# Kernel optimization log

Hardware: AMD Instinct MI355X
Metric: run time of the kernel (lower is better)

Reference implementation:

```python
import jax, jax.numpy as jnp
import numpy as np

# QConv2D (AngleMap feature map, entanglement-free PQC model):
# each 3x3 patch value x_q is angle-encoded as RY(w_q * x_q) on qubit q,
# then n_layers of trainable RZ(a)/RY(b) rotations are applied; the layer
# outputs the Bloch vector (<X>,<Y>,<Z>) of every qubit -> 3*n_qubits values
# per patch. Channel outputs are summed (Add), filters concatenated, relu.

KERNEL = (3, 3)
STRIDE = (1, 1)


def _extract_patches(x, k, s):
    # x: (B,H,W,C) -> (B,i0,i1,C,K) with K = k0*k1
    B, H, W, C = x.shape
    i0 = (H - k[0]) // s[0] + 1
    i1 = (W - k[1]) // s[1] + 1
    ri = jnp.arange(i0)[:, None] * s[0] + jnp.arange(k[0])[None, :]  # (i0,k0)
    rj = jnp.arange(i1)[:, None] * s[1] + jnp.arange(k[1])[None, :]  # (i1,k1)
    p = x[:, ri]            # (B,i0,k0,W,C)
    p = p[:, :, :, rj]      # (B,i0,k0,i1,k1,C)
    p = jnp.transpose(p, (0, 1, 3, 5, 2, 4))  # (B,i0,i1,C,k0,k1)
    return p.reshape(B, i0, i1, C, k[0] * k[1])


def setup_inputs() -> dict:
    key = jax.random.key(0)
    k_x, k_w, k_a, k_b = jax.random.split(key, 4)
    B, H, W, C = 32, 128, 128, 3
    F, Q, L = 2, KERNEL[0] * KERNEL[1], 2  # filters, n_qubits, n_layers
    input_tensor = jax.random.uniform(k_x, (B, H, W, C), dtype=jnp.float32)
    w_enc = jax.random.normal(k_w, (F, C, Q), dtype=jnp.float32)
    a_rz = jax.random.normal(k_a, (F, C, L, Q), dtype=jnp.float32)
    b_ry = jax.random.normal(k_b, (F, C, L, Q), dtype=jnp.float32)
    return {"input_tensor": input_tensor, "w_enc": w_enc, "a_rz": a_rz, "b_ry": b_ry}


def reference(input_tensor, w_enc, a_rz, b_ry):
    B = input_tensor.shape[0]
    F, C, Q = w_enc.shape
    L = a_rz.shape[2]
    patches = _extract_patches(input_tensor, KERNEL, STRIDE)  # (B,i0,i1,C,Q)
    i0, i1 = patches.shape[1], patches.shape[2]
    # angle encoding per (filter, channel, qubit)
    theta = patches[:, :, :, None, :, :] * w_enc[None, None, None]  # (B,i0,i1,F,C,Q)
    vx, vy, vz = jnp.sin(theta), jnp.zeros_like(theta), jnp.cos(theta)
    for l in range(L):  # small fixed layer count
        ca, sa = jnp.cos(a_rz[:, :, l]), jnp.sin(a_rz[:, :, l])  # (F,C,Q)
        cb, sb = jnp.cos(b_ry[:, :, l]), jnp.sin(b_ry[:, :, l])
        # RZ(a): rotate Bloch vector about Z
        vx, vy = vx * ca - vy * sa, vx * sa + vy * ca
        # RY(b): rotate about Y
        vx, vz = vx * cb + vz * sb, -vx * sb + vz * cb
    out = jnp.stack([vx, vy, vz], axis=-1)       # (B,i0,i1,F,C,Q,3)
    out = out.sum(axis=4)                        # Add over channels -> (B,i0,i1,F,Q,3)
    out = out.reshape(B, i0, i1, F * Q * 3)      # Concatenate over filters
    return jax.nn.relu(out)
```

## Files before the change

kernel.cpp:

```cpp
#include <hip/hip_runtime.h>
#include <math.h>

#define NB 32
#define NH 128
#define NW 128
#define NC 3
#define NF 2
#define NQ 9
#define NL 2
#define I0 126
#define I1 126
#define NGJ 14
#define NGROUPS (NB * I0 * NGJ)
#define GTHREADS (NGROUPS * 18)
#define INV2PI 0.15915494309189535f

struct f3 { float x, y, z; };

__global__ __launch_bounds__(256) void qconv_fused(
        const float* __restrict__ x,
        const float* __restrict__ w_enc,
        const float* __restrict__ a_rz,
        const float* __restrict__ b_ry,
        float* __restrict__ out) {
    __shared__ float stab[54 * 8];
    int tid = threadIdx.x;
    if (tid < 54) {
        int t = tid;
        int f = t / 27;
        int c = (t / 9) % 3;
        int q = t % 9;
        float ux = 1.f, uy = 0.f, uz = 0.f;
        float wx = 0.f, wy = 0.f, wz = 1.f;
#pragma unroll
        for (int l = 0; l < NL; ++l) {
            int ia = ((f * NC + c) * NL + l) * NQ + q;
            float sa, ca, sb, cb;
            __sincosf(a_rz[ia], &sa, &ca);
            __sincosf(b_ry[ia], &sb, &cb);
            float nx, ny, nz;
            nx = ux * ca - uy * sa; ny = ux * sa + uy * ca; ux = nx; uy = ny;
            nx = ux * cb + uz * sb; nz = -ux * sb + uz * cb; ux = nx; uz = nz;
            nx = wx * ca - wy * sa; ny = wx * sa + wy * ca; wx = nx; wy = ny;
            nx = wx * cb + wz * sb; nz = -wx * sb + wz * cb; wx = nx; wz = nz;
        }
        float* o = stab + t * 8;
        o[0] = w_enc[t] * INV2PI;
        o[1] = ux; o[2] = uy; o[3] = uz;
        o[4] = wx; o[5] = wy; o[6] = wz;
        o[7] = 0.f;
    }
    __syncthreads();

    int T0 = blockIdx.x * 256 + tid;
    int grp = T0 / 18;
    int q18 = T0 - grp * 18;
    int f = (q18 >= 9) ? 1 : 0;
    int q = q18 - f * 9;
    int di = q / 3, dj = q - di * 3;

    float cw[3], sx[3], sy[3], sz[3], cx[3], cy[3], cz[3];
#pragma unroll
    for (int c = 0; c < 3; ++c) {
        const float* r = stab + (size_t)(f * 27 + c * 9 + q) * 8;
        float4 v0 = *reinterpret_cast<const float4*>(r);
        float4 v1 = *reinterpret_cast<const float4*>(r + 4);
        cw[c] = v0.x; sx[c] = v0.y; sy[c] = v0.z; sz[c] = v0.w;
        cx[c] = v1.x; cy[c] = v1.y; cz[c] = v1.z;
    }

    int b   = grp / (I0 * NGJ);
    int rem = grp - b * (I0 * NGJ);
    int i   = rem / NGJ;
    int j   = (rem - i * NGJ) * 9;

    const float* pin = x + ((size_t)((b * NH + i + di) * NW) + (j + dj)) * NC;
    float* pout = out + (size_t)grp * 486 + q18 * 3;

    float p[27];
#pragma unroll
    for (int t = 0; t < 9; ++t) {
        f3 v = *reinterpret_cast<const f3*>(pin + t * 3);
        p[3 * t + 0] = v.x; p[3 * t + 1] = v.y; p[3 * t + 2] = v.z;
    }

#pragma unroll
    for (int t = 0; t < 9; ++t) {
        float a0 = 0.f, a1 = 0.f, a2 = 0.f;
#pragma unroll
        for (int c = 0; c < 3; ++c) {
            float xr = p[3 * t + c] * cw[c];
            float s  = __builtin_amdgcn_sinf(xr);
            float co = __builtin_amdgcn_cosf(xr);
            a0 = fmaf(sx[c], s, fmaf(cx[c], co, a0));
            a1 = fmaf(sy[c], s, fmaf(cy[c], co, a1));
            a2 = fmaf(sz[c], s, fmaf(cz[c], co, a2));
        }
        f3 r;
        r.x = fmaxf(a0, 0.f);
        r.y = fmaxf(a1, 0.f);
        r.z = fmaxf(a2, 0.f);
        *reinterpret_cast<f3*>(pout + t * 54) = r;
    }
}

extern "C" void kernel_launch(void* const* d_in, const int* in_sizes, int n_in,
                              void* d_out, int out_size, void* d_ws, size_t ws_size,
                              hipStream_t stream) {
    const float* x     = (const float*)d_in[0];
    const float* w_enc = (const float*)d_in[1];
    const float* a_rz  = (const float*)d_in[2];
    const float* b_ry  = (const float*)d_in[3];
    float* out = (float*)d_out;

    int block = 256;
    int grid = GTHREADS / block;
    qconv_fused<<<grid, block, 0, stream>>>(x, w_enc, a_rz, b_ry, out);
}
```

Before: 27.02 us.

## Stage outputs in shared memory and write coalesced nontemporal float4 stores

Reorganizes the thread mapping so each 576-thread block handles 128 output pixels. Each thread owns one (filter,qubit) pair and computes 4 pixels, then writes its results to shared memory. After a barrier, the block writes the contiguous output tile with float4 nontemporal stores. The goal is to replace strided 12-byte scattered writes with fully coalesced wide stores. In exchange, input reads become per-pixel strided loads, and the kernel adds shared-memory traffic and a block barrier.

```diff
diff --git a/kernel.cpp b/kernel.cpp
--- a/kernel.cpp
+++ b/kernel.cpp
@@ -10,20 +10,24 @@
 #define NL 2
 #define I0 126
 #define I1 126
-#define NGJ 14
-#define NGROUPS (NB * I0 * NGJ)
-#define GTHREADS (NGROUPS * 18)
+#define NPIX (NB * I0 * I1)
+#define PPB 128
+#define TPB 576
+#define NBLK (NPIX / PPB)
 #define INV2PI 0.15915494309189535f
 
 struct f3 { float x, y, z; };
+typedef float f4 __attribute__((ext_vector_type(4)));
 
-__global__ __launch_bounds__(256) void qconv_fused(
+__global__ __launch_bounds__(TPB) void qconv_fused(
         const float* __restrict__ x,
         const float* __restrict__ w_enc,
         const float* __restrict__ a_rz,
         const float* __restrict__ b_ry,
         float* __restrict__ out) {
     __shared__ float stab[54 * 8];
+    __shared__ float sout[PPB * 54];
+
     int tid = threadIdx.x;
     if (tid < 54) {
         int t = tid;
@@ -52,9 +56,8 @@
     }
     __syncthreads();
 
-    int T0 = blockIdx.x * 256 + tid;
-    int grp = T0 / 18;
-    int q18 = T0 - grp * 18;
+    int q18 = tid >> 5;
+    int pxl = tid & 31;
     int f = (q18 >= 9) ? 1 : 0;
     int q = q18 - f * 9;
     int di = q / 3, dj = q - di * 3;
@@ -69,38 +72,43 @@
         cx[c] = v1.x; cy[c] = v1.y; cz[c] = v1.z;
     }
 
-    int b   = grp / (I0 * NGJ);
-    int rem = grp - b * (I0 * NGJ);
-    int i   = rem / NGJ;
-    int j   = (rem - i * NGJ) * 9;
-
-    const float* pin = x + ((size_t)((b * NH + i + di) * NW) + (j + dj)) * NC;
-    float* pout = out + (size_t)grp * 486 + q18 * 3;
-
-    float p[27];
-#pragma unroll
-    for (int t = 0; t < 9; ++t) {
-        f3 v = *reinterpret_cast<const f3*>(pin + t * 3);
-        p[3 * t + 0] = v.x; p[3 * t + 1] = v.y; p[3 * t + 2] = v.z;
-    }
+    int pixbase = blockIdx.x * PPB;
 
 #pragma unroll
-    for (int t = 0; t < 9; ++t) {
+    for (int k = 0; k < 4; ++k) {
+        int px  = pixbase + pxl + 32 * k;
+        int b   = px / (I0 * I1);
+        int rem = px - b * (I0 * I1);
+        int i   = rem / I1;
+        int j   = rem - i * I1;
+
+        const float* pp = x + ((size_t)((b * NH + i + di) * NW) + (j + dj)) * NC;
+        f3 P = *reinterpret_cast<const f3*>(pp);
+
         float a0 = 0.f, a1 = 0.f, a2 = 0.f;
 #pragma unroll
         for (int c = 0; c < 3; ++c) {
-            float xr = p[3 * t + c] * cw[c];
+            float pc = (c == 0) ? P.x : (c == 1) ? P.y : P.z;
+            float xr = pc * cw[c];
             float s  = __builtin_amdgcn_sinf(xr);
             float co = __builtin_amdgcn_cosf(xr);
             a0 = fmaf(sx[c], s, fmaf(cx[c], co, a0));
             a1 = fmaf(sy[c], s, fmaf(cy[c], co, a1));
             a2 = fmaf(sz[c], s, fmaf(cz[c], co, a2));
         }
-        f3 r;
-        r.x = fmaxf(a0, 0.f);
-        r.y = fmaxf(a1, 0.f);
-        r.z = fmaxf(a2, 0.f);
-        *reinterpret_cast<f3*>(pout + t * 54) = r;
+
+        float* so = sout + (size_t)(pxl + 32 * k) * 54 + q18 * 3;
+        so[0] = fmaxf(a0, 0.f);
+        so[1] = fmaxf(a1, 0.f);
+        so[2] = fmaxf(a2, 0.f);
+    }
+    __syncthreads();
+
+    const f4* s4 = reinterpret_cast<const f4*>(sout);
+    f4* o4 = reinterpret_cast<f4*>(out + (size_t)pixbase * 54);
+#pragma unroll
+    for (int m = 0; m < 3; ++m) {
+        __builtin_nontemporal_store(s4[tid * 3 + m], o4 + tid * 3 + m);
     }
 }
 
@@ -113,7 +121,5 @@
     const float* b_ry  = (const float*)d_in[3];
     float* out = (float*)d_out;
 
-    int block = 256;
-    int grid = GTHREADS / block;
-    qconv_fused<<<grid, block, 0, stream>>>(x, w_enc, a_rz, b_ry, out);
+    qconv_fused<<<NBLK, TPB, 0, stream>>>(x, w_enc, a_rz, b_ry, out);
 }
```

New measurement: 102.0 us. +277.5%, slower.
